# Kernel tuning notes

Measured on AMD Instinct MI355X. Metric: run time of the kernel, lower is better.

Reference implementation:

```python
import jax, jax.numpy as jnp
import numpy as np

B, S, D_IN, D_H, D_OUT = 4, 2048, 512, 512, 512


def setup_inputs() -> dict:
    key = jax.random.key(0)
    ks = jax.random.split(key, 11)
    s_in = 1.0 / np.sqrt(D_IN)
    s_cat = 1.0 / np.sqrt(3 * D_H)
    return {
        "x1": jax.random.normal(ks[0], (B, S, D_IN), jnp.float32),
        "x2": jax.random.normal(ks[1], (B, S, D_IN), jnp.float32),
        "x3": jax.random.normal(ks[2], (B, S, D_IN), jnp.float32),
        "Wq": jax.random.normal(ks[3], (D_IN, D_H), jnp.float32) * s_in,
        "bq": jnp.zeros((D_H,), jnp.float32),
        "Wk": jax.random.normal(ks[4], (D_IN, D_H), jnp.float32) * s_in,
        "bk": jnp.zeros((D_H,), jnp.float32),
        "Wv": jax.random.normal(ks[5], (D_IN, D_H), jnp.float32) * s_in,
        "bv": jnp.zeros((D_H,), jnp.float32),
        "Wo": jax.random.normal(ks[6], (3 * D_H, D_OUT), jnp.float32) * s_cat,
        "bo": jnp.zeros((D_OUT,), jnp.float32),
    }


def _attn(Q, K, V):
    # Q: [B,S,H], K/V: [B,S,H] -> [B,S,H]
    scale = 1.0 / jnp.sqrt(jnp.asarray(K.shape[-1], Q.dtype))
    scores = jnp.einsum('bqh,bkh->bqk', Q, K) * scale
    w = jax.nn.softmax(scores, axis=-1)
    return jnp.einsum('bqk,bkh->bqh', w, V)


def reference(x1, x2, x3, Wq, bq, Wk, bk, Wv, bv, Wo, bo):
    Q1, Q2, Q3 = x1 @ Wq + bq, x2 @ Wq + bq, x3 @ Wq + bq
    K1, K2, K3 = x1 @ Wk + bk, x2 @ Wk + bk, x3 @ Wk + bk
    V1, V2, V3 = x1 @ Wv + bv, x2 @ Wv + bv, x3 @ Wv + bv
    fused_x1 = _attn(Q1, K2, V2) + _attn(Q1, K3, V3)
    fused_x2 = _attn(Q2, K1, V1) + _attn(Q2, K3, V3)
    fused_x3 = _attn(Q3, K1, V1) + _attn(Q3, K2, V2)
    fused = jnp.concatenate([fused_x1, fused_x2, fused_x3], axis=-1)
    return fused @ Wo + bo
```

## Files before the change

kernel.cpp:

```cpp
#include <hip/hip_runtime.h>
#include <hip/hip_bf16.h>

typedef __attribute__((ext_vector_type(4))) float  f32x4;
typedef __attribute__((ext_vector_type(8))) short  short8;

#define GAS(p) ((const __attribute__((address_space(1))) void*)(p))
#define LAS(p) ((__attribute__((address_space(3))) void*)(p))

__device__ inline short bf16_of(float f) {
    union { float f; unsigned u; } v; v.f = f;
    unsigned r = v.u + 0x7FFFu + ((v.u >> 16) & 1u);
    return (short)(r >> 16);
}

#define MFMA __builtin_amdgcn_mfma_f32_16x16x32_bf16

__device__ __forceinline__ void stage64(const short* A, long lda,
                                        const short* B, long ldb,
                                        short* As, short* Bs) {
    const int tid = threadIdx.x;
    const int w = tid >> 6, l = tid & 63;
    const int r = l >> 3;
    const int scol = ((l & 7) ^ r) * 8;
#pragma unroll
    for (int q = 0; q < 4; ++q) {
        const int rowb = q * 32 + w * 8;
        __builtin_amdgcn_global_load_lds(GAS(A + (long)(rowb + r) * lda + scol),
                                         LAS(As + rowb * 64), 16, 0, 0);
        __builtin_amdgcn_global_load_lds(GAS(B + (long)(rowb + r) * ldb + scol),
                                         LAS(Bs + rowb * 64), 16, 0, 0);
    }
}

__device__ __forceinline__ void gemm_core64(const short* A, long lda,
                                            const short* B, long ldb, int nk,
                                            short* sA, short* sB,
                                            f32x4 acc[4][4]) {
    const int tid = threadIdx.x;
    const int lane = tid & 63, wid = tid >> 6;
    const int wr = wid >> 1, wc = wid & 1;
    const int fr = lane & 15, fk = lane >> 4;
    const int swz = (fr & 7) << 4;
    const int abase = (wr * 64 + fr) * 128 + fk * 16;
    const int bbase = (wc * 64 + fr) * 128 + fk * 16;

    stage64(A, lda, B, ldb, sA, sB);
    __syncthreads();
    for (int ks = 0; ks < nk; ++ks) {
        const int cur = ks & 1;
        if (ks + 1 < nk)
            stage64(A + (ks + 1) * 64, lda, B + (ks + 1) * 64, ldb,
                    sA + (cur ^ 1) * 8192, sB + (cur ^ 1) * 8192);
        const char* pa = (const char*)(sA + cur * 8192);
        const char* pb = (const char*)(sB + cur * 8192);
        short8 af[2][4], bfr[2][4];
#pragma unroll
        for (int kk = 0; kk < 2; ++kk) {
#pragma unroll
            for (int mi = 0; mi < 4; ++mi)
                af[kk][mi] = *(const short8*)(pa + (((abase + kk * 64) ^ swz) + mi * 2048));
#pragma unroll
            for (int ni = 0; ni < 4; ++ni)
                bfr[kk][ni] = *(const short8*)(pb + (((bbase + kk * 64) ^ swz) + ni * 2048));
        }
#pragma unroll
        for (int kk = 0; kk < 2; ++kk)
#pragma unroll
            for (int mi = 0; mi < 4; ++mi)
#pragma unroll
                for (int ni = 0; ni < 4; ++ni)
                    acc[mi][ni] = MFMA(af[kk][mi], bfr[kk][ni], acc[mi][ni], 0, 0, 0);
        __syncthreads();
    }
}

__device__ __forceinline__ void bounce_store(short* Pb, const short vals[4][4][4],
                                             short* C, long ldc) {
    const int tid = threadIdx.x, lane = tid & 63, wid = tid >> 6;
    const int wr = wid >> 1, wc = wid & 1, fr = lane & 15, fk = lane >> 4;
#pragma unroll
    for (int mi = 0; mi < 4; ++mi)
#pragma unroll
        for (int ni = 0; ni < 4; ++ni)
#pragma unroll
            for (int r = 0; r < 4; ++r) {
                const int row = wr * 64 + mi * 16 + fk * 4 + r;
                const int col = wc * 64 + ni * 16 + fr;
                Pb[row * 128 + (col ^ ((row & 7) << 3))] = vals[mi][ni][r];
            }
    __syncthreads();
#pragma unroll
    for (int i = 0; i < 8; ++i) {
        const int row = i * 16 + (tid >> 4);
        const int ch = tid & 15;
        short8 v = *(const short8*)&Pb[row * 128 + ((ch * 8) ^ ((row & 7) << 3))];
        *(short8*)&C[(long)row * ldc + ch * 8] = v;
    }
}

__global__ __launch_bounds__(256, 2)
void proj_qk_k(const short* __restrict__ xb, const short* __restrict__ WqkT,
               short* __restrict__ Qb, short* __restrict__ Kb,
               const float* __restrict__ bq, const float* __restrict__ bk) {
    __shared__ short sA[2 * 8192], sB[2 * 8192];
    const short* Ab = xb + (long)blockIdx.x * 128 * 512;
    const short* Bb = WqkT + (long)blockIdx.y * 128 * 512;
    f32x4 acc[4][4] = {};
    gemm_core64(Ab, 512, Bb, 512, 8, sA, sB, acc);

    const int lane = threadIdx.x & 63, wid = threadIdx.x >> 6;
    const int wc = wid & 1, fr = lane & 15;
    const int qc0 = blockIdx.y * 128;
    const float* bias = qc0 < 512 ? bq + qc0 : bk + (qc0 - 512);
    short vals[4][4][4];
#pragma unroll
    for (int mi = 0; mi < 4; ++mi)
#pragma unroll
        for (int ni = 0; ni < 4; ++ni) {
            const float bv_ = bias[wc * 64 + ni * 16 + fr];
#pragma unroll
            for (int r = 0; r < 4; ++r)
                vals[mi][ni][r] = bf16_of(acc[mi][ni][r] + bv_);
        }
    short* dst = (qc0 < 512 ? Qb + qc0 : Kb + (qc0 - 512)) + (long)blockIdx.x * 128 * 512;
    bounce_store(sA, vals, dst, 512);
}

__global__ __launch_bounds__(256, 2)
void proj_vt_k(const short* __restrict__ WvT, const short* __restrict__ xb,
               short* __restrict__ VT, const float* __restrict__ bv) {
    __shared__ short sA[2 * 8192], sB[2 * 8192];
    const short* Ab = WvT + (long)blockIdx.x * 128 * 512;
    const short* Bb = xb + (long)blockIdx.y * 128 * 512;
    f32x4 acc[4][4] = {};
    gemm_core64(Ab, 512, Bb, 512, 8, sA, sB, acc);

    const int lane = threadIdx.x & 63, wid = threadIdx.x >> 6;
    const int wr = wid >> 1, fk = lane >> 4;
    short vals[4][4][4];
#pragma unroll
    for (int mi = 0; mi < 4; ++mi)
#pragma unroll
        for (int ni = 0; ni < 4; ++ni)
#pragma unroll
            for (int r = 0; r < 4; ++r) {
                const int rowg = blockIdx.x * 128 + wr * 64 + mi * 16 + fk * 4 + r;
                vals[mi][ni][r] = bf16_of(acc[mi][ni][r] + bv[rowg]);
            }
    bounce_store(sA, vals, VT + (long)blockIdx.x * 128 * 24576 + blockIdx.y * 128, 24576);
}

struct Off6 { long a[6], b[6]; };

__global__ __launch_bounds__(256, 2)
void qk_exp(const short* __restrict__ Qb, const short* __restrict__ Kb,
            short* __restrict__ Sc, float* __restrict__ lpart,
            Off6 o, int z0, int zmask, int zshift, float kscale) {
    __shared__ short sA[2 * 8192], sB[2 * 8192];
    const int bid = blockIdx.x;
    const int z = bid & zmask;
    const int t = bid >> zshift;
    const int bx = t & 15, by = t >> 4;
    const int slice = z0 + z;
    const int gp = slice >> 2, b = slice & 3;
    const short* Ab = Qb + o.a[gp] + ((long)b * 2048 + (long)bx * 128) * 512;
    const short* Bb = Kb + o.b[gp] + ((long)b * 2048 + (long)by * 128) * 512;
    f32x4 acc[4][4] = {};
    gemm_core64(Ab, 512, Bb, 512, 8, sA, sB, acc);

    const int tid = threadIdx.x, lane = tid & 63, wid = tid >> 6;
    const int wr = wid >> 1, wc = wid & 1, fr = lane & 15, fk = lane >> 4;

#pragma unroll
    for (int mi = 0; mi < 4; ++mi)
#pragma unroll
        for (int ni = 0; ni < 4; ++ni)
#pragma unroll
            for (int r = 0; r < 4; ++r)
                acc[mi][ni][r] = exp2f(acc[mi][ni][r] * kscale);

#pragma unroll
    for (int mi = 0; mi < 4; ++mi)
#pragma unroll
        for (int r = 0; r < 4; ++r) {
            float s = acc[mi][0][r] + acc[mi][1][r] + acc[mi][2][r] + acc[mi][3][r];
            s += __shfl_xor(s, 1); s += __shfl_xor(s, 2);
            s += __shfl_xor(s, 4); s += __shfl_xor(s, 8);
            if (fr == 0)
                lpart[((long)z * 32 + by * 2 + wc) * 2048 +
                      (long)bx * 128 + wr * 64 + mi * 16 + fk * 4 + r] = s;
        }

    short vals[4][4][4];
#pragma unroll
    for (int mi = 0; mi < 4; ++mi)
#pragma unroll
        for (int ni = 0; ni < 4; ++ni)
#pragma unroll
            for (int r = 0; r < 4; ++r)
                vals[mi][ni][r] = bf16_of(acc[mi][ni][r]);

    short* Cb = Sc + (long)z * 2048 * 2048 +
                (long)bx * 128 * 2048 + (long)by * 128;
    bounce_store(sA, vals, Cb, 2048);
}

struct POff { long v[6], c[6]; };

__global__ __launch_bounds__(256, 2)
void pv_div(const short* __restrict__ Sc, const short* __restrict__ VT,
            const float* __restrict__ lpart, short* __restrict__ F,
            POff o, int z0, int zmask, int zshift) {
    __shared__ short sA[2 * 8192], sB[2 * 8192];
    const int bid = blockIdx.x;
    const int z = bid & zmask;
    const int t = bid >> zshift;
    const int bx = t & 15, by = t >> 4;
    const int slice = z0 + z;
    const int gp = slice >> 2, b = slice & 3;
    const short* Ab = Sc + (long)z * 2048 * 2048 + (long)bx * 128 * 2048;
    const short* Bb = VT + o.v[gp] + (long)b * 2048 + (long)by * 128 * 24576;
    f32x4 acc[4][4] = {};
    gemm_core64(Ab, 2048, Bb, 24576, 32, sA, sB, acc);

    const int tid = threadIdx.x, lane = tid & 63, wid = tid >> 6;
    const int wr = wid >> 1, wc = wid & 1, fr = lane & 15, fk = lane >> 4;

    float* linv_s = (float*)sB;
    if (tid < 128) {
        const float* lp = lpart + ((long)z * 32) * 2048 + (long)bx * 128 + tid;
        float s = 0.f;
#pragma unroll
        for (int j = 0; j < 32; ++j) s += lp[(long)j * 2048];
        linv_s[tid] = 1.0f / s;
    }
    __syncthreads();

    short vals[4][4][4];
#pragma unroll
    for (int mi = 0; mi < 4; ++mi) {
        float linv[4];
#pragma unroll
        for (int r = 0; r < 4; ++r) linv[r] = linv_s[wr * 64 + mi * 16 + fk * 4 + r];
#pragma unroll
        for (int ni = 0; ni < 4; ++ni)
#pragma unroll
            for (int r = 0; r < 4; ++r)
                vals[mi][ni][r] = bf16_of(acc[mi][ni][r] * linv[r]);
    }
    __syncthreads();

    short* Cb = F + ((long)b * 2048 + (long)bx * 128) * 3072 +
                o.c[gp] + (long)by * 128;
    bounce_store(sA, vals, Cb, 3072);
}

__global__ __launch_bounds__(256, 2)
void final_f32(const short* __restrict__ A, const short* __restrict__ B,
               float* __restrict__ C, const float* __restrict__ bias) {
    __shared__ short sA[2 * 8192], sB[2 * 8192];
    const short* Ab = A + (long)blockIdx.x * 128 * 3072;
    const short* Bb = B + (long)blockIdx.y * 128 * 3072;
    f32x4 acc[4][4] = {};
    gemm_core64(Ab, 3072, Bb, 3072, 48, sA, sB, acc);

    const int lane = threadIdx.x & 63, wid = threadIdx.x >> 6;
    const int wr = wid >> 1, wc = wid & 1, fr = lane & 15, fk = lane >> 4;
    const long r0 = (long)blockIdx.x * 128 + wr * 64 + fk * 4;
    const long c0 = (long)blockIdx.y * 128 + wc * 64 + fr;
#pragma unroll
    for (int mi = 0; mi < 4; ++mi)
#pragma unroll
        for (int ni = 0; ni < 4; ++ni) {
            const long rr = r0 + mi * 16, cc = c0 + ni * 16;
#pragma unroll
            for (int r = 0; r < 4; ++r)
                C[(rr + r) * 512 + cc] = acc[mi][ni][r] + bias[cc];
        }
}

__global__ __launch_bounds__(256)
void xconv(const float* __restrict__ x0, const float* __restrict__ x1,
           const float* __restrict__ x2, short* __restrict__ xb) {
    const float* s = blockIdx.z == 0 ? x0 : (blockIdx.z == 1 ? x1 : x2);
    const long i = ((long)blockIdx.x * 256 + threadIdx.x) * 8;
    f32x4 a = *(const f32x4*)(s + i), c = *(const f32x4*)(s + i + 4);
    short8 v;
    v[0] = bf16_of(a.x); v[1] = bf16_of(a.y); v[2] = bf16_of(a.z); v[3] = bf16_of(a.w);
    v[4] = bf16_of(c.x); v[5] = bf16_of(c.y); v[6] = bf16_of(c.z); v[7] = bf16_of(c.w);
    *(short8*)(xb + (long)blockIdx.z * 8192 * 512 + i) = v;
}

__global__ __launch_bounds__(256)
void wprep(const float* __restrict__ Wq, const float* __restrict__ Wk,
           const float* __restrict__ Wv, const float* __restrict__ Wo,
           short* __restrict__ WqkT, short* __restrict__ WvT,
           short* __restrict__ WoT2) {
    __shared__ float t[32][33];
    const int z = blockIdx.z;
    const float* src; short* dst; int rows; long ldd; bool dup = false;
    if (z == 0)      { src = Wq; dst = WqkT;              rows = 512;  ldd = 512; }
    else if (z == 1) { src = Wk; dst = WqkT + 512L * 512; rows = 512;  ldd = 512; }
    else if (z == 2) { src = Wv; dst = WvT;               rows = 512;  ldd = 512; }
    else             { src = Wo; dst = WoT2;              rows = 1536; ldd = 3072; dup = true; }
    const int r0 = blockIdx.x * 32, c0 = blockIdx.y * 32;
    if (r0 >= rows) return;
    const int lx = threadIdx.x & 31, ly = threadIdx.x >> 5;
#pragma unroll
    for (int p = 0; p < 4; ++p)
        t[ly + 8 * p][lx] = src[(long)(r0 + ly + 8 * p) * 512 + (c0 + lx)];
    __syncthreads();
#pragma unroll
    for (int p = 0; p < 4; ++p) {
        const short v = bf16_of(t[lx][ly + 8 * p]);
        const long base = (long)(c0 + ly + 8 * p) * ldd + (r0 + lx);
        dst[base] = v;
        if (dup) dst[base + 1536] = v;
    }
}

extern "C" void kernel_launch(void* const* d_in, const int* in_sizes, int n_in,
                              void* d_out, int out_size, void* d_ws, size_t ws_size,
                              hipStream_t stream) {
    const float* x[3] = { (const float*)d_in[0], (const float*)d_in[1], (const float*)d_in[2] };
    const float* Wq = (const float*)d_in[3]; const float* bq = (const float*)d_in[4];
    const float* Wk = (const float*)d_in[5]; const float* bk = (const float*)d_in[6];
    const float* Wv = (const float*)d_in[7]; const float* bv = (const float*)d_in[8];
    const float* Wo = (const float*)d_in[9]; const float* bo = (const float*)d_in[10];

    const long TOK = 8192, T3 = 3 * TOK;

    char* ws = (char*)d_ws;
    size_t off = 0;
    auto alloc = [&](size_t bytes) -> void* {
        void* pp = ws + off;
        off += (bytes + 255) & ~(size_t)255;
        return pp;
    };

    short* WqkT  = (short*)alloc(1024L * 512 * 2);
    short* WvT   = (short*)alloc(512L * 512 * 2);
    short* WoT2  = (short*)alloc(512L * 3072 * 2);
    short* Qb    = (short*)alloc(T3 * 512 * 2);
    short* Kb    = (short*)alloc(T3 * 512 * 2);
    short* VT    = (short*)alloc(512L * T3 * 2);
    short* fused = (short*)alloc(TOK * 3072 * 2);
    float* lpart = (float*)alloc(8L * 32 * 2048 * 4);
    short* xb    = (short*)alloc(T3 * 512 * 2);

    const size_t SLICE = 2048L * 2048 * 2;
    const size_t rem = ws_size > off ? ws_size - off : 0;
    const int nsl = (rem >= 8 * SLICE) ? 8 : 4;
    const int zshift = (nsl == 8) ? 3 : 2;
    short* scores = (short*)alloc((size_t)nsl * SLICE);

    const dim3 tb(256);
    wprep<<<dim3(48, 16, 4), tb, 0, stream>>>(Wq, Wk, Wv, Wo, WqkT, WvT, WoT2);
    xconv<<<dim3(2048, 1, 3), tb, 0, stream>>>(x[0], x[1], x[2], xb);

    proj_qk_k<<<dim3(192, 8), tb, 0, stream>>>(xb, WqkT, Qb, Kb, bq, bk);
    proj_vt_k<<<dim3(4, 192), tb, 0, stream>>>(WvT, xb, VT, bv);

    const int imap[6] = {0, 1, 2, 0, 1, 2};
    const int jmap[6] = {1, 0, 0, 2, 2, 1};
    Off6 qo{}; POff po{};
    for (int gp = 0; gp < 6; ++gp) {
        qo.a[gp] = (long)imap[gp] * TOK * 512;
        qo.b[gp] = (long)jmap[gp] * TOK * 512;
        po.v[gp] = (long)jmap[gp] * TOK;
        po.c[gp] = (long)imap[gp] * 512 + (gp >= 3 ? 1536 : 0);
    }
    const float kscale = 0.04419417382415922f * 1.4426950408889634f;

    for (int z0 = 0; z0 < 24; z0 += nsl) {
        qk_exp<<<dim3(256 * nsl), tb, 0, stream>>>(Qb, Kb, scores, lpart, qo,
                                                   z0, nsl - 1, zshift, kscale);
        pv_div<<<dim3(64 * nsl), tb, 0, stream>>>(scores, VT, lpart, fused, po,
                                                  z0, nsl - 1, zshift);
    }

    final_f32<<<dim3(64, 4), tb, 0, stream>>>(fused, WoT2, (float*)d_out, bo);
}
```

Before: 427.3 us.

## Replace QK score GEMM with 256x256 tile, 8-wave pipelined kernel

```diff
diff --git a/kernel.cpp b/kernel.cpp
--- a/kernel.cpp
+++ b/kernel.cpp
@@ -98,6 +98,117 @@
     }
 }
 
+__device__ __forceinline__ void stage_slab(const short* G, long ld, short* slab) {
+    const int w = threadIdx.x >> 6, l = threadIdx.x & 63;
+    const int rr = l >> 3, ch = l & 7;
+#pragma unroll
+    for (int q = 0; q < 4; ++q) {
+        const int row = q * 64 + w * 8 + rr;
+        __builtin_amdgcn_global_load_lds(GAS(G + (long)row * ld + ((ch ^ (row & 7)) * 8)),
+                                         LAS(slab + (q * 64 + w * 8) * 64), 16, 0, 0);
+    }
+}
+
+__device__ __forceinline__ short8 lds_frag(const short* slab, int row, int c) {
+    return *(const short8*)((const char*)slab + row * 128 + ((c ^ (row & 7)) * 16));
+}
+
+#define PH_FENCE asm volatile("" ::: "memory")
+
+template<int KK, int MH, bool RB>
+__device__ __forceinline__ void phase_block(const short* a, const short* b,
+                                            int wm, int wn, int fr, int fk,
+                                            short8 (&bf)[4], f32x4 (&acc)[8][4]) {
+    short8 af[4];
+#pragma unroll
+    for (int m = 0; m < 4; ++m)
+        af[m] = lds_frag(a, wm * 128 + MH * 64 + m * 16 + fr, KK * 4 + fk);
+    if (RB) {
+#pragma unroll
+        for (int n = 0; n < 4; ++n)
+            bf[n] = lds_frag(b, wn * 64 + n * 16 + fr, KK * 4 + fk);
+    }
+    PH_FENCE; __builtin_amdgcn_s_barrier();
+    asm volatile("s_waitcnt lgkmcnt(0)" ::: "memory");
+    __builtin_amdgcn_sched_barrier(0);
+    __builtin_amdgcn_s_setprio(1);
+#pragma unroll
+    for (int m = 0; m < 4; ++m)
+#pragma unroll
+        for (int n = 0; n < 4; ++n)
+            acc[MH * 4 + m][n] = MFMA(af[m], bf[n], acc[MH * 4 + m][n], 0, 0, 0);
+    __builtin_amdgcn_s_setprio(0);
+    PH_FENCE; __builtin_amdgcn_s_barrier(); PH_FENCE;
+}
+
+template<int KK, int MH>
+__device__ __forceinline__ void phase3_block(const short* a, const short* Bg, long ldb,
+                                             short* stage_dst, bool do_stage,
+                                             int wm, int wn, int fr, int fk,
+                                             short8 (&bf)[4], f32x4 (&acc)[8][4]) {
+    short8 af[4];
+#pragma unroll
+    for (int m = 0; m < 4; ++m)
+        af[m] = lds_frag(a, wm * 128 + MH * 64 + m * 16 + fr, KK * 4 + fk);
+    if (do_stage) {
+        stage_slab(Bg, ldb, stage_dst);
+        asm volatile("s_waitcnt vmcnt(4)" ::: "memory");
+    } else {
+        asm volatile("s_waitcnt vmcnt(0)" ::: "memory");
+    }
+    __builtin_amdgcn_sched_barrier(0);
+    PH_FENCE; __builtin_amdgcn_s_barrier();
+    asm volatile("s_waitcnt lgkmcnt(0)" ::: "memory");
+    __builtin_amdgcn_sched_barrier(0);
+    __builtin_amdgcn_s_setprio(1);
+#pragma unroll
+    for (int m = 0; m < 4; ++m)
+#pragma unroll
+        for (int n = 0; n < 4; ++n)
+            acc[MH * 4 + m][n] = MFMA(af[m], bf[n], acc[MH * 4 + m][n], 0, 0, 0);
+    __builtin_amdgcn_s_setprio(0);
+    PH_FENCE; __builtin_amdgcn_s_barrier(); PH_FENCE;
+}
+
+__device__ __forceinline__ void gemm256_core(const short* Ag, long lda,
+                                             const short* Bg, long ldb, int nk,
+                                             short* lds, f32x4 (&acc)[8][4]) {
+    short* sA = lds;
+    short* sB = lds + 32768;
+    const int tid = threadIdx.x, lane = tid & 63, w = tid >> 6;
+    const int wm = w >> 2, wn = w & 3, fr = lane & 15, fk = lane >> 4;
+
+    stage_slab(Bg, ldb, sB);
+    stage_slab(Ag, lda, sA);
+    stage_slab(Bg + 64, ldb, sB + 16384);
+    asm volatile("s_waitcnt vmcnt(4)" ::: "memory");
+    __builtin_amdgcn_sched_barrier(0);
+    PH_FENCE; __builtin_amdgcn_s_barrier(); PH_FENCE;
+
+    short8 bf[4];
+    for (int t = 0; t < nk; ++t) {
+        const short* a = sA + (t & 1) * 16384;
+        const short* b = sB + (t & 1) * 16384;
+        if (t + 1 < nk)
+            stage_slab(Ag + (long)(t + 1) * 64, lda, sA + ((t + 1) & 1) * 16384);
+        phase_block<0, 0, true >(a, b, wm, wn, fr, fk, bf, acc);
+        phase_block<0, 1, false>(a, b, wm, wn, fr, fk, bf, acc);
+        phase_block<1, 0, true >(a, b, wm, wn, fr, fk, bf, acc);
+        phase3_block<1, 1>(a, Bg + (long)(t + 2) * 64, ldb, sB + (t & 1) * 16384,
+                           t + 2 < nk, wm, wn, fr, fk, bf, acc);
+    }
+}
+
+__device__ __forceinline__ void wave_tile_store(const short* wbuf, short* Cw, long ldc) {
+    const int l = threadIdx.x & 63, rr = l >> 3, ch = l & 7;
+#pragma unroll
+    for (int p = 0; p < 16; ++p) {
+        const int row = p * 8 + rr;
+        short8 v = *(const short8*)((const char*)wbuf + row * 128 + ((ch ^ (row & 7)) * 16));
+        *(short8*)&Cw[(long)row * ldc + ch * 8] = v;
+    }
+}
+
 __global__ __launch_bounds__(256, 2)
 void proj_qk_k(const short* __restrict__ xb, const short* __restrict__ WqkT,
                short* __restrict__ Qb, short* __restrict__ Kb,
@@ -152,57 +263,57 @@
 
 struct Off6 { long a[6], b[6]; };
 
-__global__ __launch_bounds__(256, 2)
-void qk_exp(const short* __restrict__ Qb, const short* __restrict__ Kb,
-            short* __restrict__ Sc, float* __restrict__ lpart,
-            Off6 o, int z0, int zmask, int zshift, float kscale) {
-    __shared__ short sA[2 * 8192], sB[2 * 8192];
+__global__ __launch_bounds__(512, 2)
+void qk256(const short* __restrict__ Qb, const short* __restrict__ Kb,
+           short* __restrict__ Sc, float* __restrict__ lpart,
+           Off6 o, int z0, float kscale) {
+    __shared__ short lds[65536];
     const int bid = blockIdx.x;
-    const int z = bid & zmask;
-    const int t = bid >> zshift;
-    const int bx = t & 15, by = t >> 4;
+    const int z = bid & 7;
+    const int t = bid >> 3;
+    const int bx = t & 7, by = t >> 3;
     const int slice = z0 + z;
     const int gp = slice >> 2, b = slice & 3;
-    const short* Ab = Qb + o.a[gp] + ((long)b * 2048 + (long)bx * 128) * 512;
-    const short* Bb = Kb + o.b[gp] + ((long)b * 2048 + (long)by * 128) * 512;
-    f32x4 acc[4][4] = {};
-    gemm_core64(Ab, 512, Bb, 512, 8, sA, sB, acc);
-
-    const int tid = threadIdx.x, lane = tid & 63, wid = tid >> 6;
-    const int wr = wid >> 1, wc = wid & 1, fr = lane & 15, fk = lane >> 4;
-
-#pragma unroll
-    for (int mi = 0; mi < 4; ++mi)
-#pragma unroll
-        for (int ni = 0; ni < 4; ++ni)
+    const short* Ag = Qb + o.a[gp] + ((long)b * 2048 + (long)bx * 256) * 512;
+    const short* Bg = Kb + o.b[gp] + ((long)b * 2048 + (long)by * 256) * 512;
+    f32x4 acc[8][4] = {};
+    gemm256_core(Ag, 512, Bg, 512, 8, lds, acc);
+
+    const int tid = threadIdx.x, lane = tid & 63, w = tid >> 6;
+    const int wm = w >> 2, wn = w & 3, fr = lane & 15, fk = lane >> 4;
+
+#pragma unroll
+    for (int m = 0; m < 8; ++m)
+#pragma unroll
+        for (int n = 0; n < 4; ++n)
 #pragma unroll
             for (int r = 0; r < 4; ++r)
-                acc[mi][ni][r] = exp2f(acc[mi][ni][r] * kscale);
-
-#pragma unroll
-    for (int mi = 0; mi < 4; ++mi)
+                acc[m][n][r] = exp2f(acc[m][n][r] * kscale);
+
+    float* lp = lpart + ((long)z * 32 + by * 4 + wn) * 2048 + (long)bx * 256 + wm * 128;
+#pragma unroll
+    for (int m = 0; m < 8; ++m)
 #pragma unroll
         for (int r = 0; r < 4; ++r) {
-            float s = acc[mi][0][r] + acc[mi][1][r] + acc[mi][2][r] + acc[mi][3][r];
+            float s = acc[m][0][r] + acc[m][1][r] + acc[m][2][r] + acc[m][3][r];
             s += __shfl_xor(s, 1); s += __shfl_xor(s, 2);
             s += __shfl_xor(s, 4); s += __shfl_xor(s, 8);
-            if (fr == 0)
-                lpart[((long)z * 32 + by * 2 + wc) * 2048 +
-                      (long)bx * 128 + wr * 64 + mi * 16 + fk * 4 + r] = s;
+            if (fr == 0) lp[m * 16 + fk * 4 + r] = s;
         }
 
-    short vals[4][4][4];
-#pragma unroll
-    for (int mi = 0; mi < 4; ++mi)
-#pragma unroll
-        for (int ni = 0; ni < 4; ++ni)
-#pragma unroll
-            for (int r = 0; r < 4; ++r)
-                vals[mi][ni][r] = bf16_of(acc[mi][ni][r]);
-
-    short* Cb = Sc + (long)z * 2048 * 2048 +
-                (long)bx * 128 * 2048 + (long)by * 128;
-    bounce_store(sA, vals, Cb, 2048);
+    short* wbuf = lds + w * 8192;
+#pragma unroll
+    for (int m = 0; m < 8; ++m)
+#pragma unroll
+        for (int n = 0; n < 4; ++n)
+#pragma unroll
+            for (int r = 0; r < 4; ++r) {
+                const int row = m * 16 + fk * 4 + r, col = n * 16 + fr;
+                *(short*)((char*)wbuf + ((row * 128 + col * 2) ^ ((row & 7) << 4))) = bf16_of(acc[m][n][r]);
+            }
+    short* Cw = Sc + (long)z * 2048 * 2048 + ((long)bx * 256 + wm * 128) * 2048
+                + by * 256 + wn * 64;
+    wave_tile_store(wbuf, Cw, 2048);
 }
 
 struct POff { long v[6], c[6]; };
@@ -210,11 +321,11 @@
 __global__ __launch_bounds__(256, 2)
 void pv_div(const short* __restrict__ Sc, const short* __restrict__ VT,
             const float* __restrict__ lpart, short* __restrict__ F,
-            POff o, int z0, int zmask, int zshift) {
+            POff o, int z0) {
     __shared__ short sA[2 * 8192], sB[2 * 8192];
     const int bid = blockIdx.x;
-    const int z = bid & zmask;
-    const int t = bid >> zshift;
+    const int z = bid & 7;
+    const int t = bid >> 3;
     const int bx = t & 15, by = t >> 4;
     const int slice = z0 + z;
     const int gp = slice >> 2, b = slice & 3;
@@ -347,12 +458,7 @@
     short* fused = (short*)alloc(TOK * 3072 * 2);
     float* lpart = (float*)alloc(8L * 32 * 2048 * 4);
     short* xb    = (short*)alloc(T3 * 512 * 2);
-
-    const size_t SLICE = 2048L * 2048 * 2;
-    const size_t rem = ws_size > off ? ws_size - off : 0;
-    const int nsl = (rem >= 8 * SLICE) ? 8 : 4;
-    const int zshift = (nsl == 8) ? 3 : 2;
-    short* scores = (short*)alloc((size_t)nsl * SLICE);
+    short* scores = (short*)alloc(8L * 2048 * 2048 * 2);
 
     const dim3 tb(256);
     wprep<<<dim3(48, 16, 4), tb, 0, stream>>>(Wq, Wk, Wv, Wo, WqkT, WvT, WoT2);
@@ -372,11 +478,9 @@
     }
     const float kscale = 0.04419417382415922f * 1.4426950408889634f;
 
-    for (int z0 = 0; z0 < 24; z0 += nsl) {
-        qk_exp<<<dim3(256 * nsl), tb, 0, stream>>>(Qb, Kb, scores, lpart, qo,
-                                                   z0, nsl - 1, zshift, kscale);
-        pv_div<<<dim3(64 * nsl), tb, 0, stream>>>(scores, VT, lpart, fused, po,
-                                                  z0, nsl - 1, zshift);
+    for (int z0 = 0; z0 < 24; z0 += 8) {
+        qk256<<<dim3(512), dim3(512), 0, stream>>>(Qb, Kb, scores, lpart, qo, z0, kscale);
+        pv_div<<<dim3(512), tb, 0, stream>>>(scores, VT, lpart, fused, po, z0);
     }
 
     final_f32<<<dim3(64, 4), tb, 0, stream>>>(fused, WoT2, (float*)d_out, bo);
```

Result: faster. 416.8 us (-2.5%).

## Use 128x64 output tiles in final projection GEMM for more blocks

Applied to the files above, without the earlier changes.

```diff
diff --git a/kernel.cpp b/kernel.cpp
--- a/kernel.cpp
+++ b/kernel.cpp
@@ -255,21 +255,69 @@
     bounce_store(sA, vals, Cb, 3072);
 }
 
-__global__ __launch_bounds__(256, 2)
-void final_f32(const short* __restrict__ A, const short* __restrict__ B,
-               float* __restrict__ C, const float* __restrict__ bias) {
-    __shared__ short sA[2 * 8192], sB[2 * 8192];
+__device__ __forceinline__ void stage_f(const short* A, const short* B,
+                                        short* As, short* Bs) {
+    const int tid = threadIdx.x, w = tid >> 6, l = tid & 63;
+    const int r = l >> 3, scol = ((l & 7) ^ r) * 8;
+#pragma unroll
+    for (int q = 0; q < 4; ++q) {
+        const int rowb = q * 32 + w * 8;
+        __builtin_amdgcn_global_load_lds(GAS(A + (long)(rowb + r) * 3072 + scol),
+                                         LAS(As + rowb * 64), 16, 0, 0);
+    }
+#pragma unroll
+    for (int q = 0; q < 2; ++q) {
+        const int rowb = q * 32 + w * 8;
+        __builtin_amdgcn_global_load_lds(GAS(B + (long)(rowb + r) * 3072 + scol),
+                                         LAS(Bs + rowb * 64), 16, 0, 0);
+    }
+}
+
+__global__ __launch_bounds__(256, 3)
+void final64(const short* __restrict__ A, const short* __restrict__ B,
+             float* __restrict__ C, const float* __restrict__ bias) {
+    __shared__ short sA[2 * 8192], sB[2 * 4096];
     const short* Ab = A + (long)blockIdx.x * 128 * 3072;
-    const short* Bb = B + (long)blockIdx.y * 128 * 3072;
-    f32x4 acc[4][4] = {};
-    gemm_core64(Ab, 3072, Bb, 3072, 48, sA, sB, acc);
-
-    const int lane = threadIdx.x & 63, wid = threadIdx.x >> 6;
-    const int wr = wid >> 1, wc = wid & 1, fr = lane & 15, fk = lane >> 4;
-    const long r0 = (long)blockIdx.x * 128 + wr * 64 + fk * 4;
-    const long c0 = (long)blockIdx.y * 128 + wc * 64 + fr;
-#pragma unroll
-    for (int mi = 0; mi < 4; ++mi)
+    const short* Bb = B + (long)blockIdx.y * 64 * 3072;
+    const int tid = threadIdx.x, lane = tid & 63, w = tid >> 6;
+    const int fr = lane & 15, fk = lane >> 4;
+    const int swz = (fr & 7) << 4;
+    const int abase = (w * 32 + fr) * 128 + fk * 16;
+    const int bbase = fr * 128 + fk * 16;
+
+    f32x4 acc[2][4] = {};
+    stage_f(Ab, Bb, sA, sB);
+    __syncthreads();
+    for (int ks = 0; ks < 48; ++ks) {
+        const int cur = ks & 1;
+        if (ks + 1 < 48)
+            stage_f(Ab + (ks + 1) * 64, Bb + (ks + 1) * 64,
+                    sA + (cur ^ 1) * 8192, sB + (cur ^ 1) * 4096);
+        const char* pa = (const char*)(sA + cur * 8192);
+        const char* pb = (const char*)(sB + cur * 4096);
+        short8 af[2][2], bf[2][4];
+#pragma unroll
+        for (int kk = 0; kk < 2; ++kk) {
+#pragma unroll
+            for (int mi = 0; mi < 2; ++mi)
+                af[kk][mi] = *(const short8*)(pa + (((abase + kk * 64) ^ swz) + mi * 2048));
+#pragma unroll
+            for (int ni = 0; ni < 4; ++ni)
+                bf[kk][ni] = *(const short8*)(pb + (((bbase + kk * 64) ^ swz) + ni * 2048));
+        }
+#pragma unroll
+        for (int kk = 0; kk < 2; ++kk)
+#pragma unroll
+            for (int mi = 0; mi < 2; ++mi)
+#pragma unroll
+                for (int ni = 0; ni < 4; ++ni)
+                    acc[mi][ni] = MFMA(af[kk][mi], bf[kk][ni], acc[mi][ni], 0, 0, 0);
+        __syncthreads();
+    }
+    const long r0 = (long)blockIdx.x * 128 + w * 32 + fk * 4;
+    const long c0 = (long)blockIdx.y * 64 + fr;
+#pragma unroll
+    for (int mi = 0; mi < 2; ++mi)
 #pragma unroll
         for (int ni = 0; ni < 4; ++ni) {
             const long rr = r0 + mi * 16, cc = c0 + ni * 16;
@@ -379,5 +427,5 @@
                                                   z0, nsl - 1, zshift);
     }
 
-    final_f32<<<dim3(64, 4), tb, 0, stream>>>(fused, WoT2, (float*)d_out, bo);
-}
+    final64<<<dim3(64, 8), tb, 0, stream>>>(fused, WoT2, (float*)d_out, bo);
+}
```

New measurement: 415.4 us. -2.8%, faster.
